# Performance work log

Measured on AMD Instinct MI355X. Metric: run time of the kernel, lower is better.

## Reference

```python
import jax, jax.numpy as jnp
import numpy as np
from jax.ops import segment_sum, segment_max

G_GRAPHS = 64  # number of graphs for global_mean_pool
H_ATTN = 4     # GPSConv global attention heads


def _bn(h, g, b, eps=1e-5):
    # BatchNorm1d over nodes, training-mode (biased) batch statistics
    mu = h.mean(0)
    var = ((h - mu) ** 2).mean(0)
    return (h - mu) * jax.lax.rsqrt(var + eps) * g + b


def _forward(x, edge_index, batch, pre_w1, pre_b1, pre_w2, pre_b2,
             gat_wl, gat_bl, gat_wr, gat_br, gat_att, gat_bias,
             attn_in_w, attn_in_b, attn_out_w, attn_out_b,
             bn1_g, bn1_b, bn2_g, bn2_b, bn3_g, bn3_b,
             mlp_w1, mlp_b1, mlp_w2, mlp_b2, fin_w, fin_b):
    N = x.shape[0]
    L = gat_wl.shape[0]
    loops = jnp.arange(N)
    src = jnp.concatenate([edge_index[0], loops])  # GATv2Conv add_self_loops=True
    dst = jnp.concatenate([edge_index[1], loops])

    # preprocess MLP (exact GELU, as torch.nn.GELU default)
    x = jax.nn.gelu(x @ pre_w1 + pre_b1, approximate=False)
    x = jax.nn.gelu(x @ pre_w2 + pre_b2, approximate=False)

    for l in range(L):
        D = x.shape[1]
        dh = D // H_ATTN
        # ---- local GATv2Conv (heads=1, concat) ----
        xl = x @ gat_wl[l] + gat_bl[l]  # source transform
        xr = x @ gat_wr[l] + gat_br[l]  # target transform
        e = jax.nn.leaky_relu(xl[src] + xr[dst], 0.2) @ gat_att[l]  # [E]
        m = segment_max(e, dst, num_segments=N)
        a = jnp.exp(e - m[dst])
        s = segment_sum(a, dst, num_segments=N)
        alpha = a / s[dst]
        h1 = segment_sum(alpha[:, None] * xl[src], dst, num_segments=N) + gat_bias[l]
        h1 = _bn(h1 + x, bn1_g[l], bn1_b[l])  # residual + norm1
        # ---- global multi-head self-attention over all N nodes (batch=None) ----
        qkv = x @ attn_in_w[l].T + attn_in_b[l]
        q, k, v = jnp.split(qkv, 3, axis=-1)
        q = q.reshape(N, H_ATTN, dh).transpose(1, 0, 2)  # [H,N,dh]
        k = k.reshape(N, H_ATTN, dh).transpose(1, 0, 2)
        v = v.reshape(N, H_ATTN, dh).transpose(1, 0, 2)
        probs = jax.nn.softmax(jnp.einsum('hnd,hmd->hnm', q, k) / np.sqrt(dh), axis=-1)
        o = jnp.einsum('hnm,hmd->hnd', probs, v).transpose(1, 0, 2).reshape(N, D)
        h2 = o @ attn_out_w[l].T + attn_out_b[l]
        h2 = _bn(h2 + x, bn2_g[l], bn2_b[l])  # residual + norm2
        # ---- combine + MLP + norm3 ----
        out = h1 + h2
        out = out + (jax.nn.relu(out @ mlp_w1[l] + mlp_b1[l]) @ mlp_w2[l] + mlp_b2[l])
        out = _bn(out, bn3_g[l], bn3_b[l])
        x = jax.nn.relu(out)  # outer F.relu; dropout is identity in eval

    # global_mean_pool
    sums = segment_sum(x, batch, num_segments=G_GRAPHS)
    cnt = jnp.maximum(segment_sum(jnp.ones((N,), x.dtype), batch, num_segments=G_GRAPHS), 1.0)
    logits = (sums / cnt[:, None]) @ fin_w + fin_b
    return jax.nn.log_softmax(logits, axis=-1)


def setup_inputs() -> dict:
    N, E, F_IN, D, C, L = 4096, 262144, 9, 64, 10, 3
    key = jax.random.key(0)
    ks = iter(jax.random.split(key, 64))
    def nrm(shape, fan):
        return jax.random.normal(next(ks), shape, jnp.float32) / np.sqrt(fan)
    def zeros(shape):
        return jnp.zeros(shape, jnp.float32)
    x = jax.random.normal(next(ks), (N, F_IN), jnp.float32)
    edge_index = jax.random.randint(next(ks), (2, E), 0, N)
    batch = jnp.sort(jax.random.randint(next(ks), (N,), 0, G_GRAPHS))
    return dict(
        x=x, edge_index=edge_index, batch=batch,
        pre_w1=nrm((F_IN, 2 * D), F_IN), pre_b1=zeros((2 * D,)),
        pre_w2=nrm((2 * D, D), 2 * D), pre_b2=zeros((D,)),
        gat_wl=nrm((L, D, D), D), gat_bl=zeros((L, D)),
        gat_wr=nrm((L, D, D), D), gat_br=zeros((L, D)),
        gat_att=nrm((L, D), D), gat_bias=zeros((L, D)),
        attn_in_w=nrm((L, 3 * D, D), D), attn_in_b=zeros((L, 3 * D)),
        attn_out_w=nrm((L, D, D), D), attn_out_b=zeros((L, D)),
        bn1_g=jnp.ones((L, D), jnp.float32), bn1_b=zeros((L, D)),
        bn2_g=jnp.ones((L, D), jnp.float32), bn2_b=zeros((L, D)),
        bn3_g=jnp.ones((L, D), jnp.float32), bn3_b=zeros((L, D)),
        mlp_w1=nrm((L, D, 2 * D), D), mlp_b1=zeros((L, 2 * D)),
        mlp_w2=nrm((L, 2 * D, D), 2 * D), mlp_b2=zeros((L, D)),
        fin_w=nrm((D, C), D), fin_b=zeros((C,)),
    )


def reference(x, edge_index, batch, pre_w1, pre_b1, pre_w2, pre_b2,
              gat_wl, gat_bl, gat_wr, gat_br, gat_att, gat_bias,
              attn_in_w, attn_in_b, attn_out_w, attn_out_b,
              bn1_g, bn1_b, bn2_g, bn2_b, bn3_g, bn3_b,
              mlp_w1, mlp_b1, mlp_w2, mlp_b2, fin_w, fin_b):
    return _forward(x, edge_index, batch, pre_w1, pre_b1, pre_w2, pre_b2,
                    gat_wl, gat_bl, gat_wr, gat_br, gat_att, gat_bias,
                    attn_in_w, attn_in_b, attn_out_w, attn_out_b,
                    bn1_g, bn1_b, bn2_g, bn2_b, bn3_g, bn3_b,
                    mlp_w1, mlp_b1, mlp_w2, mlp_b2, fin_w, fin_b)
```

## Files before the change

kernel.cpp:

```cpp
#include <hip/hip_runtime.h>
#include <math.h>

#define N_NODE 4096
#define N_EDGE 262144
#define E_TOT (N_EDGE + N_NODE)
#define DD 64
#define NL 3
#define NG 64

typedef __fp16 h2_t __attribute__((ext_vector_type(2)));
union H2x4 { uint4 u; h2_t h[4]; };

__device__ __forceinline__ void atomAddF(float* p, float v) {
#if defined(__HIP_PLATFORM_AMD__)
  unsafeAtomicAdd(p, v);
#else
  atomicAdd(p, v);
#endif
}

__global__ void csr_count_kernel(const int* __restrict__ ei, int* __restrict__ cnt) {
  int e = blockIdx.x * blockDim.x + threadIdx.x;
  if (e >= E_TOT) return;
  int dst = (e < N_EDGE) ? ei[N_EDGE + e] : (e - N_EDGE);
  atomicAdd(&cnt[dst], 1);
}

__global__ void csr_scan_kernel(const int* __restrict__ cnt, int* __restrict__ row_ptr,
                                int* __restrict__ nextp) {
  __shared__ int ps[256];
  __shared__ int ps2[257];
  int t = threadIdx.x;
  int base = t * 16;
  int loc[16];
  int s = 0;
#pragma unroll
  for (int k = 0; k < 16; ++k) { loc[k] = s; s += cnt[base + k]; }
  ps[t] = s;
  __syncthreads();
  if (t == 0) {
    int a = 0;
    for (int u = 0; u < 256; ++u) { ps2[u] = a; a += ps[u]; }
    ps2[256] = a;
  }
  __syncthreads();
  int off = ps2[t];
#pragma unroll
  for (int k = 0; k < 16; ++k) {
    int v = off + loc[k];
    row_ptr[base + k] = v;
    nextp[base + k] = v;
  }
  if (t == 0) row_ptr[N_NODE] = ps2[256];
}

__global__ void csr_fill_kernel(const int* __restrict__ ei, int* __restrict__ nextp,
                                int* __restrict__ csr_src) {
  int e = blockIdx.x * blockDim.x + threadIdx.x;
  if (e >= E_TOT) return;
  int src, dst;
  if (e < N_EDGE) { src = ei[e]; dst = ei[N_EDGE + e]; }
  else { src = dst = e - N_EDGE; }
  int pos = atomicAdd(&nextp[dst], 1);
  csr_src[pos] = src;
}

__global__ void build_w_kernel(const float* __restrict__ wl, const float* __restrict__ bl,
                               const float* __restrict__ wr, const float* __restrict__ br,
                               const float* __restrict__ win, const float* __restrict__ bin,
                               const float* __restrict__ wout,
                               float* __restrict__ cw, float* __restrict__ cbias,
                               float* __restrict__ tout) {
  int idx = blockIdx.x * blockDim.x + threadIdx.x;
  if (idx < NL * 64 * 320) {
    int l = idx / 20480, rem = idx % 20480;
    int k = rem / 320, j = rem % 320;
    float v;
    if (j < 64) v = wl[l * 4096 + k * 64 + j];
    else if (j < 128) v = wr[l * 4096 + k * 64 + (j - 64)];
    else v = win[l * 12288 + (j - 128) * 64 + k];
    cw[idx] = v;
  }
  if (idx < NL * 320) {
    int l = idx / 320, j = idx % 320;
    float v;
    if (j < 64) v = bl[l * 64 + j];
    else if (j < 128) v = br[l * 64 + (j - 64)];
    else v = bin[l * 192 + (j - 128)];
    cbias[idx] = v;
  }
  if (idx < NL * 4096) {
    int l = idx / 4096, rem = idx % 4096;
    int k = rem / 64, j = rem % 64;
    tout[l * 4096 + k * 64 + j] = wout[l * 4096 + j * 64 + k];
  }
}

__global__ void linear_kernel(const float* __restrict__ A, const float* __restrict__ W,
                              const float* __restrict__ bias, float* __restrict__ C,
                              float* __restrict__ C2, int split,
                              const float* __restrict__ resid,
                              int K, int Nc, int act) {
  extern __shared__ float sA[];
  int R = blockDim.x / Nc;
  int r = threadIdx.x / Nc;
  int j = threadIdx.x - r * Nc;
  int row0 = blockIdx.x * R;
  for (int idx = threadIdx.x; idx < R * K; idx += blockDim.x)
    sA[idx] = A[row0 * K + idx];
  __syncthreads();
  int row = row0 + r;
  const float* a = sA + r * K;
  float acc = bias[j];
#pragma unroll 8
  for (int k = 0; k < K; ++k) acc = fmaf(a[k], W[k * Nc + j], acc);
  if (act == 1) acc = 0.5f * acc * (1.0f + erff(acc * 0.70710678118654752f));
  else if (act == 2) acc = fmaxf(acc, 0.0f);
  if (resid) acc += resid[row * Nc + j];
  if (j < split) C[row * split + j] = acc;
  else C2[row * (Nc - split) + (j - split)] = acc;
}

__global__ void gat_agg_kernel(const float* __restrict__ x, const float* __restrict__ xlr,
                               const float* __restrict__ att, const float* __restrict__ gbias,
                               const int* __restrict__ row_ptr, const int* __restrict__ csr_src,
                               float* __restrict__ z1) {
  int wave = (blockIdx.x * blockDim.x + threadIdx.x) >> 6;
  int lane = threadIdx.x & 63;
  if (wave >= N_NODE) return;
  int i = wave;
  float xr_d = xlr[i * 128 + 64 + lane];
  float att_d = att[lane];
  float m = -INFINITY, s = 0.f, acc = 0.f;
  int e0 = row_ptr[i], e1 = row_ptr[i + 1];
  for (int e = e0; e < e1; ++e) {
    int src = csr_src[e];
    float xl_d = xlr[src * 128 + lane];
    float v = xl_d + xr_d;
    float lr = (v > 0.f) ? v : 0.2f * v;
    float p = lr * att_d;
#pragma unroll
    for (int off = 32; off; off >>= 1) p += __shfl_xor(p, off, 64);
    float nm = fmaxf(m, p);
    float corr = __expf(m - nm);
    float w = __expf(p - nm);
    s = s * corr + w;
    acc = acc * corr + w * xl_d;
    m = nm;
  }
  z1[i * DD + lane] = x[i * DD + lane] + gbias[lane] + acc / s;
}

__global__ void colstats_kernel(const float* __restrict__ z, float* __restrict__ stats) {
  int d = threadIdx.x & 63;
  int rg = threadIdx.x >> 6;
  int i0 = blockIdx.x * 128;
  float s = 0.f, q = 0.f;
  for (int i = i0 + rg; i < i0 + 128; i += 4) {
    float v = z[i * DD + d];
    s += v;
    q += v * v;
  }
  atomAddF(&stats[d], s);
  atomAddF(&stats[64 + d], q);
}

__global__ void bn_apply_kernel(const float* __restrict__ z, const float* __restrict__ stats,
                                const float* __restrict__ g, const float* __restrict__ b,
                                float* __restrict__ out, int relu) {
  int idx = blockIdx.x * blockDim.x + threadIdx.x;
  if (idx >= N_NODE * DD) return;
  int d = idx & 63;
  const float invN = 1.0f / (float)N_NODE;
  float mu = stats[d] * invN;
  float var = stats[64 + d] * invN - mu * mu;
  float rstd = rsqrtf(var + 1e-5f);
  float v = (z[idx] - mu) * rstd * g[d] + b[d];
  if (relu) v = fmaxf(v, 0.f);
  out[idx] = v;
}

__global__ void bnbn_kernel(const float* __restrict__ z1, const float* __restrict__ st1,
                            const float* __restrict__ g1, const float* __restrict__ b1,
                            const float* __restrict__ z2, const float* __restrict__ st2,
                            const float* __restrict__ g2, const float* __restrict__ b2,
                            float* __restrict__ comb) {
  int idx = blockIdx.x * blockDim.x + threadIdx.x;
  if (idx >= N_NODE * DD) return;
  int d = idx & 63;
  const float invN = 1.0f / (float)N_NODE;
  float mu1 = st1[d] * invN;
  float v1 = st1[64 + d] * invN - mu1 * mu1;
  float h1 = (z1[idx] - mu1) * rsqrtf(v1 + 1e-5f) * g1[d] + b1[d];
  float mu2 = st2[d] * invN;
  float v2 = st2[64 + d] * invN - mu2 * mu2;
  float h2 = (z2[idx] - mu2) * rsqrtf(v2 + 1e-5f) * g2[d] + b2[d];
  comb[idx] = h1 + h2;
}

__global__ void knorm_kernel(const float* __restrict__ qkv, int* __restrict__ kmax) {
  __shared__ int lmax[4];
  int tid = threadIdx.x;
  if (tid < 4) lmax[tid] = 0;
  __syncthreads();
  int idx = blockIdx.x * 256 + tid;
  int j = idx >> 2, h = idx & 3;
  const float* kr = qkv + (size_t)j * 192 + 64 + h * 16;
  float n2 = 0.f;
#pragma unroll
  for (int c = 0; c < 16; ++c) { float v = kr[c]; n2 = fmaf(v, v, n2); }
  atomicMax(&lmax[h], __float_as_int(sqrtf(n2)));
  __syncthreads();
  if (tid < 4) atomicMax(&kmax[tid], lmax[tid]);
}

#define TJ 256
__global__ void attn_kernel(const float* __restrict__ qkv, const int* __restrict__ kmax,
                            float* __restrict__ accS, float* __restrict__ accO) {
  __shared__ __align__(16) float smem[4416];
  uint4* kt = (uint4*)smem;
  uint4* vt = (uint4*)(smem + 2048);
  int h = blockIdx.y, js = blockIdx.z;
  int i0 = blockIdx.x * 64;
  int r = threadIdx.x & 63;
  int gq = threadIdx.x >> 6;
  int i = i0 + r;
  float qf[16];
  const float* qr = qkv + (size_t)i * 192 + h * 16;
#pragma unroll
  for (int c = 0; c < 16; ++c) qf[c] = qr[c] * 0.25f;
  float qn2 = 0.f;
#pragma unroll
  for (int c = 0; c < 16; ++c) qn2 = fmaf(qf[c], qf[c], qn2);
  float m = sqrtf(qn2) * __int_as_float(kmax[h]);
  h2_t q2[8];
#pragma unroll
  for (int c = 0; c < 8; ++c) q2[c] = __builtin_amdgcn_cvt_pkrtz(qf[2 * c], qf[2 * c + 1]);
  float s = 0.f;
  float acc[16];
#pragma unroll
  for (int c = 0; c < 16; ++c) acc[c] = 0.f;

  for (int t = 0; t < 2; ++t) {
    int j0 = js * 512 + t * TJ;
    __syncthreads();
    {
      int jj = threadIdx.x;
      const float* kr = qkv + (size_t)(j0 + jj) * 192 + 64 + h * 16;
      float4 a = *(const float4*)kr, b = *(const float4*)(kr + 4);
      float4 c4f = *(const float4*)(kr + 8), d4 = *(const float4*)(kr + 12);
      H2x4 w0, w1;
      w0.h[0] = __builtin_amdgcn_cvt_pkrtz(a.x, a.y); w0.h[1] = __builtin_amdgcn_cvt_pkrtz(a.z, a.w);
      w0.h[2] = __builtin_amdgcn_cvt_pkrtz(b.x, b.y); w0.h[3] = __builtin_amdgcn_cvt_pkrtz(b.z, b.w);
      w1.h[0] = __builtin_amdgcn_cvt_pkrtz(c4f.x, c4f.y); w1.h[1] = __builtin_amdgcn_cvt_pkrtz(c4f.z, c4f.w);
      w1.h[2] = __builtin_amdgcn_cvt_pkrtz(d4.x, d4.y); w1.h[3] = __builtin_amdgcn_cvt_pkrtz(d4.z, d4.w);
      kt[jj * 2] = w0.u; kt[jj * 2 + 1] = w1.u;
      for (int id = threadIdx.x; id < 512; id += 256) {
        int c4 = id & 3, jp = id >> 2;
        const float* va = qkv + (size_t)(j0 + 2 * jp) * 192 + 128 + h * 16 + c4 * 4;
        float4 A = *(const float4*)va, B = *(const float4*)(va + 192);
        H2x4 w;
        w.h[0] = __builtin_amdgcn_cvt_pkrtz(A.x, B.x); w.h[1] = __builtin_amdgcn_cvt_pkrtz(A.y, B.y);
        w.h[2] = __builtin_amdgcn_cvt_pkrtz(A.z, B.z); w.h[3] = __builtin_amdgcn_cvt_pkrtz(A.w, B.w);
        vt[c4 * 128 + jp] = w.u;
      }
    }
    __syncthreads();
    for (int jp = gq; jp < 128; jp += 4) {
      H2x4 ka0, ka1, kb0, kb1;
      ka0.u = kt[jp * 4 + 0]; ka1.u = kt[jp * 4 + 1];
      kb0.u = kt[jp * 4 + 2]; kb1.u = kt[jp * 4 + 3];
      float sa = 0.f, sb = 0.f;
#pragma unroll
      for (int c = 0; c < 4; ++c) {
        sa = __builtin_amdgcn_fdot2(q2[c], ka0.h[c], sa, false);
        sb = __builtin_amdgcn_fdot2(q2[c], kb0.h[c], sb, false);
      }
#pragma unroll
      for (int c = 0; c < 4; ++c) {
        sa = __builtin_amdgcn_fdot2(q2[4 + c], ka1.h[c], sa, false);
        sb = __builtin_amdgcn_fdot2(q2[4 + c], kb1.h[c], sb, false);
      }
      float pa = __expf(sa - m), pb = __expf(sb - m);
      s += pa + pb;
      h2_t pp = __builtin_amdgcn_cvt_pkrtz(pa, pb);
      H2x4 v0, v1, v2, v3;
      v0.u = vt[jp]; v1.u = vt[128 + jp]; v2.u = vt[256 + jp]; v3.u = vt[384 + jp];
#pragma unroll
      for (int c = 0; c < 4; ++c) {
        acc[c]      = __builtin_amdgcn_fdot2(pp, v0.h[c], acc[c], false);
        acc[4 + c]  = __builtin_amdgcn_fdot2(pp, v1.h[c], acc[4 + c], false);
        acc[8 + c]  = __builtin_amdgcn_fdot2(pp, v2.h[c], acc[8 + c], false);
        acc[12 + c] = __builtin_amdgcn_fdot2(pp, v3.h[c], acc[12 + c], false);
      }
    }
  }
  __syncthreads();
  float* cb = smem;
  cb[(gq * 17 + 16) * 64 + r] = s;
#pragma unroll
  for (int c = 0; c < 16; ++c) cb[(gq * 17 + c) * 64 + r] = acc[c];
  __syncthreads();
  if (gq == 0) {
    float S = 0.f;
#pragma unroll
    for (int g2 = 0; g2 < 4; ++g2) S += cb[(g2 * 17 + 16) * 64 + r];
    atomAddF(&accS[h * N_NODE + i], S);
#pragma unroll
    for (int c = 0; c < 16; ++c) {
      float A = 0.f;
#pragma unroll
      for (int g2 = 0; g2 < 4; ++g2) A += cb[(g2 * 17 + c) * 64 + r];
      atomAddF(&accO[(h * 16 + c) * N_NODE + i], A);
    }
  }
}

__global__ void attn_norm_kernel(float* __restrict__ accO, float* __restrict__ accS,
                                 int* __restrict__ kmax, float* __restrict__ o) {
  int idx = blockIdx.x * 256 + threadIdx.x;
  int i = idx >> 6, d = idx & 63, h = d >> 4;
  o[idx] = accO[d * N_NODE + i] / accS[h * N_NODE + i];
  __syncthreads();
  accO[d * N_NODE + i] = 0.f;
  if ((d & 15) == 0) accS[h * N_NODE + i] = 0.f;
  if (idx < 4) kmax[idx] = 0;
}

__global__ void pool_kernel(const float* __restrict__ x, const int* __restrict__ batch,
                            float* __restrict__ pool, float* __restrict__ pcnt) {
  int idx = blockIdx.x * blockDim.x + threadIdx.x;
  if (idx >= N_NODE * DD) return;
  int i = idx >> 6, d = idx & 63;
  int g = batch[i];
  atomAddF(&pool[g * DD + d], x[idx]);
  if (d == 0) atomAddF(&pcnt[g], 1.0f);
}

__global__ void final_kernel(const float* __restrict__ pool, const float* __restrict__ pcnt,
                             const float* __restrict__ fw, const float* __restrict__ fb,
                             float* __restrict__ out) {
  int g = blockIdx.x;
  int d = threadIdx.x;
  __shared__ float mean[64];
  __shared__ float lg[16];
  float c = fmaxf(pcnt[g], 1.0f);
  mean[d] = pool[g * DD + d] / c;
  __syncthreads();
  if (d < 10) {
    float acc = fb[d];
#pragma unroll 8
    for (int k = 0; k < 64; ++k) acc += mean[k] * fw[k * 10 + d];
    lg[d] = acc;
  }
  __syncthreads();
  if (d == 0) {
    float mx = -INFINITY;
    for (int c2 = 0; c2 < 10; ++c2) mx = fmaxf(mx, lg[c2]);
    float sum = 0.f;
    for (int c2 = 0; c2 < 10; ++c2) sum += expf(lg[c2] - mx);
    lg[10] = mx + logf(sum);
  }
  __syncthreads();
  if (d < 10) out[g * 10 + d] = lg[d] - lg[10];
}

static void run_linear(const float* A, const float* W, const float* b, float* C,
                       float* C2, int split, const float* resid,
                       int K, int Nc, int act, int R, hipStream_t s) {
  int block = Nc * R;
  int grid = N_NODE / R;
  hipLaunchKernelGGL(linear_kernel, dim3(grid), dim3(block), R * K * sizeof(float), s,
                     A, W, b, C, C2, split, resid, K, Nc, act);
}

extern "C" void kernel_launch(void* const* d_in, const int* in_sizes, int n_in,
                              void* d_out, int out_size, void* d_ws, size_t ws_size,
                              hipStream_t stream) {
  const float* x_in      = (const float*)d_in[0];
  const int*   edge_idx  = (const int*)d_in[1];
  const int*   batch     = (const int*)d_in[2];
  const float* pre_w1    = (const float*)d_in[3];
  const float* pre_b1    = (const float*)d_in[4];
  const float* pre_w2    = (const float*)d_in[5];
  const float* pre_b2    = (const float*)d_in[6];
  const float* gat_wl    = (const float*)d_in[7];
  const float* gat_bl    = (const float*)d_in[8];
  const float* gat_wr    = (const float*)d_in[9];
  const float* gat_br    = (const float*)d_in[10];
  const float* gat_att   = (const float*)d_in[11];
  const float* gat_bias  = (const float*)d_in[12];
  const float* attn_in_w = (const float*)d_in[13];
  const float* attn_in_b = (const float*)d_in[14];
  const float* attn_out_w= (const float*)d_in[15];
  const float* attn_out_b= (const float*)d_in[16];
  const float* bn1_g     = (const float*)d_in[17];
  const float* bn1_b     = (const float*)d_in[18];
  const float* bn2_g     = (const float*)d_in[19];
  const float* bn2_b     = (const float*)d_in[20];
  const float* bn3_g     = (const float*)d_in[21];
  const float* bn3_b     = (const float*)d_in[22];
  const float* mlp_w1    = (const float*)d_in[23];
  const float* mlp_b1    = (const float*)d_in[24];
  const float* mlp_w2    = (const float*)d_in[25];
  const float* mlp_b2    = (const float*)d_in[26];
  const float* fin_w     = (const float*)d_in[27];
  const float* fin_b     = (const float*)d_in[28];
  float* out = (float*)d_out;

  float* ws = (float*)d_ws;
  float* xbuf  = ws;
  float* qkv   = xbuf + 262144;
  float* xlr   = qkv + 786432;
  float* hid   = xlr + 524288;
  float* obuf  = hid;
  float* z1    = hid + 262144;
  float* z2    = hid + 524288;
  float* comb  = z2 + 262144;
  float* cw    = comb + 262144;
  float* cbias = cw + 61440;
  float* tout  = cbias + 960;
  float* zr    = tout + 12288;
  int*   cnt   = (int*)zr;
  float* stats = zr + 4096;
  float* pool  = stats + 1152;
  float* pcnt  = pool + 4096;
  int*   kmax  = (int*)(pcnt + 64);
  float* accS  = (float*)(kmax + 4);
  float* accO  = accS + 16384;
  size_t zr_elems = 4096 + 1152 + 4096 + 64 + 4 + 16384 + 262144;
  float* zend  = accO + 262144;
  int* row_ptr = (int*)zend;
  int* nextp   = row_ptr + 4097;
  int* csr_src = nextp + 4096;

  hipMemsetAsync(zr, 0, zr_elems * sizeof(float), stream);

  hipLaunchKernelGGL(csr_count_kernel, dim3((E_TOT + 255) / 256), dim3(256), 0, stream,
                     edge_idx, cnt);
  hipLaunchKernelGGL(csr_scan_kernel, dim3(1), dim3(256), 0, stream, cnt, row_ptr, nextp);
  hipLaunchKernelGGL(csr_fill_kernel, dim3((E_TOT + 255) / 256), dim3(256), 0, stream,
                     edge_idx, nextp, csr_src);

  hipLaunchKernelGGL(build_w_kernel, dim3((NL * 64 * 320 + 255) / 256), dim3(256), 0, stream,
                     gat_wl, gat_bl, gat_wr, gat_br, attn_in_w, attn_in_b, attn_out_w,
                     cw, cbias, tout);

  run_linear(x_in, pre_w1, pre_b1, xlr, nullptr, 128, nullptr, 9, 128, 1, 2, stream);
  run_linear(xlr, pre_w2, pre_b2, xbuf, nullptr, 64, nullptr, 128, 64, 1, 4, stream);

  for (int l = 0; l < NL; ++l) {
    const float* attv = gat_att + l * DD;
    const float* gbias = gat_bias + l * DD;
    float* st1 = stats + (l * 3 + 0) * 128;
    float* st2 = stats + (l * 3 + 1) * 128;
    float* st3 = stats + (l * 3 + 2) * 128;

    run_linear(xbuf, cw + l * 20480, cbias + l * 320, xlr, qkv, 128, nullptr,
               64, 320, 0, 2, stream);

    hipLaunchKernelGGL(knorm_kernel, dim3(64), dim3(256), 0, stream, qkv, kmax);
    hipLaunchKernelGGL(attn_kernel, dim3(N_NODE / 64, 4, 8), dim3(256), 0, stream,
                       qkv, kmax, accS, accO);
    hipLaunchKernelGGL(attn_norm_kernel, dim3(N_NODE * DD / 256), dim3(256), 0, stream,
                       accO, accS, kmax, obuf);

    hipLaunchKernelGGL(gat_agg_kernel, dim3(N_NODE / 4), dim3(256), 0, stream,
                       xbuf, xlr, attv, gbias, row_ptr, csr_src, z1);
    hipLaunchKernelGGL(colstats_kernel, dim3(32), dim3(256), 0, stream, z1, st1);

    run_linear(obuf, tout + l * 4096, attn_out_b + l * DD, z2, nullptr, 64, xbuf,
               64, 64, 0, 4, stream);
    hipLaunchKernelGGL(colstats_kernel, dim3(32), dim3(256), 0, stream, z2, st2);

    hipLaunchKernelGGL(bnbn_kernel, dim3(N_NODE * DD / 256), dim3(256), 0, stream,
                       z1, st1, bn1_g + l * DD, bn1_b + l * DD,
                       z2, st2, bn2_g + l * DD, bn2_b + l * DD, comb);

    run_linear(comb, mlp_w1 + l * 8192, mlp_b1 + l * 128, hid, nullptr, 128, nullptr,
               64, 128, 2, 2, stream);
    run_linear(hid, mlp_w2 + l * 8192, mlp_b2 + l * DD, z2, nullptr, 64, comb,
               128, 64, 0, 4, stream);
    hipLaunchKernelGGL(colstats_kernel, dim3(32), dim3(256), 0, stream, z2, st3);
    hipLaunchKernelGGL(bn_apply_kernel, dim3(N_NODE * DD / 256), dim3(256), 0, stream,
                       z2, st3, bn3_g + l * DD, bn3_b + l * DD, xbuf, 1);
  }

  hipLaunchKernelGGL(pool_kernel, dim3(N_NODE * DD / 256), dim3(256), 0, stream,
                     xbuf, batch, pool, pcnt);
  hipLaunchKernelGGL(final_kernel, dim3(NG), dim3(64), 0, stream, pool, pcnt, fin_w, fin_b, out);
}
```

Measured before the change: 769.8 us.

## Fuse batchnorm, stats and attention normalization into templated linear kernels

Replaces the generic linear kernel with a templated one that keeps weights in registers and processes 16 rows per block. BatchNorm application is folded into the input loads and residual adds of the following linears. Column statistics become per-block partial sums plus a small reduction kernel, and the attention normalization and accumulator clearing move into the output projection. This cuts launches and full-tensor round trips through memory, at the cost of more template variants, register pressure from large weight arrays, and recomputing BN per consumer.

Measured after the change: 1.801 ms. 2.34x slower.

```diff
diff --git a/kernel.cpp b/kernel.cpp
--- a/kernel.cpp
+++ b/kernel.cpp
@@ -17,6 +17,16 @@
 #else
   atomicAdd(p, v);
 #endif
+}
+
+__device__ __forceinline__ float bn_eval(float z, const float* st, const float* g,
+                                         const float* b, int d, bool relu) {
+  if (st == nullptr) return z;
+  const float invN = 2.44140625e-4f;
+  float mu = st[d] * invN;
+  float var = fmaf(st[64 + d], invN, -mu * mu);
+  float v = (z - mu) * rsqrtf(var + 1e-5f) * g[d] + b[d];
+  return relu ? fmaxf(v, 0.f) : v;
 }
 
 __global__ void csr_count_kernel(const int* __restrict__ ei, int* __restrict__ cnt) {
@@ -96,39 +106,140 @@
   }
 }
 
-__global__ void linear_kernel(const float* __restrict__ A, const float* __restrict__ W,
-                              const float* __restrict__ bias, float* __restrict__ C,
-                              float* __restrict__ C2, int split,
-                              const float* __restrict__ resid,
-                              int K, int Nc, int act) {
-  extern __shared__ float sA[];
-  int R = blockDim.x / Nc;
-  int r = threadIdx.x / Nc;
-  int j = threadIdx.x - r * Nc;
-  int row0 = blockIdx.x * R;
-  for (int idx = threadIdx.x; idx < R * K; idx += blockDim.x)
-    sA[idx] = A[row0 * K + idx];
-  __syncthreads();
-  int row = row0 + r;
-  const float* a = sA + r * K;
-  float acc = bias[j];
-#pragma unroll 8
-  for (int k = 0; k < K; ++k) acc = fmaf(a[k], W[k * Nc + j], acc);
-  if (act == 1) acc = 0.5f * acc * (1.0f + erff(acc * 0.70710678118654752f));
-  else if (act == 2) acc = fmaxf(acc, 0.0f);
-  if (resid) acc += resid[row * Nc + j];
-  if (j < split) C[row * split + j] = acc;
-  else C2[row * (Nc - split) + (j - split)] = acc;
-}
-
-__global__ void gat_agg_kernel(const float* __restrict__ x, const float* __restrict__ xlr,
-                               const float* __restrict__ att, const float* __restrict__ gbias,
-                               const int* __restrict__ row_ptr, const int* __restrict__ csr_src,
-                               float* __restrict__ z1) {
-  int wave = (blockIdx.x * blockDim.x + threadIdx.x) >> 6;
-  int lane = threadIdx.x & 63;
-  if (wave >= N_NODE) return;
-  int i = wave;
+struct LinP {
+  const float *A, *A2, *W, *bias;
+  float *C, *C2;
+  const float *i_st, *i_g, *i_b, *i2_st, *i2_g, *i2_b;
+  const float *R, *R2, *r_st, *r_g, *r_b, *r2_st, *r2_g, *r2_b;
+  float *accO_w, *accS_w;
+  int* kmax_clr;
+  float* spart;
+};
+
+template<int NC, int KK, int TIN, int TRES, int ACT, bool SPLIT, bool STOUT, bool KCLR>
+__global__ void lin_kernel(LinP P) {
+  constexpr int BLK = (NC < 256) ? 256 : NC;
+  constexpr int G = BLK / NC;
+  constexpr int BR = 16;
+  constexpr int RPT = BR / G;
+  constexpr int LDA = (KK % 4 == 0) ? KK + 4 : KK;
+  __shared__ __align__(16) float sA[BR * LDA];
+  __shared__ float sred[4 * 128];
+  const int tid = threadIdx.x;
+  const int row0 = blockIdx.x * BR;
+
+  for (int idx = tid; idx < BR * KK; idx += BLK) {
+    int r, k;
+    if constexpr (TIN == 3) { r = idx & 15; k = idx >> 4; }
+    else { r = idx / KK; k = idx - r * KK; }
+    int row = row0 + r;
+    float v;
+    if constexpr (TIN == 0) v = P.A[row * KK + k];
+    else if constexpr (TIN == 1) v = bn_eval(P.A[row * 64 + k], P.i_st, P.i_g, P.i_b, k, true);
+    else if constexpr (TIN == 2) v = bn_eval(P.A[row * 64 + k], P.i_st, P.i_g, P.i_b, k, false)
+                                   + bn_eval(P.A2[row * 64 + k], P.i2_st, P.i2_g, P.i2_b, k, false);
+    else {
+      float num = P.accO_w[k * 4096 + row];
+      float den = P.accS_w[(k >> 4) * 4096 + row];
+      v = num / den;
+      P.accO_w[k * 4096 + row] = 0.f;
+    }
+    sA[r * LDA + k] = v;
+  }
+  if constexpr (KCLR) { if (blockIdx.x == 0 && tid < 4) P.kmax_clr[tid] = 0; }
+
+  int j, rg;
+  if constexpr (G == 1) { j = tid; rg = 0; }
+  else { j = tid & (NC - 1); rg = tid >> (NC == 64 ? 6 : 7); }
+
+  float w[KK];
+#pragma unroll
+  for (int k = 0; k < KK; ++k) w[k] = P.W[k * NC + j];
+  float bs = P.bias[j];
+  float acc[RPT];
+#pragma unroll
+  for (int rr = 0; rr < RPT; ++rr) acc[rr] = bs;
+  __syncthreads();
+
+  if constexpr (TIN == 3) {
+    if (tid < 64) P.accS_w[(tid >> 4) * 4096 + row0 + (tid & 15)] = 0.f;
+  }
+
+  if constexpr (KK % 4 == 0) {
+#pragma unroll
+    for (int rr = 0; rr < RPT; ++rr) {
+      const float* ap = sA + (rg * RPT + rr) * LDA;
+#pragma unroll
+      for (int k4 = 0; k4 < KK / 4; ++k4) {
+        float4 a = *(const float4*)(ap + 4 * k4);
+        acc[rr] = fmaf(a.x, w[4 * k4 + 0], acc[rr]);
+        acc[rr] = fmaf(a.y, w[4 * k4 + 1], acc[rr]);
+        acc[rr] = fmaf(a.z, w[4 * k4 + 2], acc[rr]);
+        acc[rr] = fmaf(a.w, w[4 * k4 + 3], acc[rr]);
+      }
+    }
+  } else {
+#pragma unroll
+    for (int rr = 0; rr < RPT; ++rr) {
+      const float* ap = sA + (rg * RPT + rr) * LDA;
+#pragma unroll
+      for (int k = 0; k < KK; ++k) acc[rr] = fmaf(ap[k], w[k], acc[rr]);
+    }
+  }
+
+  float lsum = 0.f, lsq = 0.f;
+#pragma unroll
+  for (int rr = 0; rr < RPT; ++rr) {
+    int row = row0 + rg * RPT + rr;
+    float v = acc[rr];
+    if constexpr (ACT == 1) v = 0.5f * v * (1.0f + erff(v * 0.70710678118654752f));
+    else if constexpr (ACT == 2) v = fmaxf(v, 0.0f);
+    if constexpr (TRES == 1) v += bn_eval(P.R[row * 64 + j], P.r_st, P.r_g, P.r_b, j, true);
+    else if constexpr (TRES == 2) v += bn_eval(P.R[row * 64 + j], P.r_st, P.r_g, P.r_b, j, false)
+                                     + bn_eval(P.R2[row * 64 + j], P.r2_st, P.r2_g, P.r2_b, j, false);
+    if constexpr (SPLIT) {
+      if (j < 128) P.C[row * 128 + j] = v;
+      else P.C2[row * 192 + (j - 128)] = v;
+    } else {
+      P.C[row * NC + j] = v;
+    }
+    if constexpr (STOUT) { lsum += v; lsq = fmaf(v, v, lsq); }
+  }
+  if constexpr (STOUT) {
+    sred[rg * 128 + j] = lsum;
+    sred[rg * 128 + 64 + j] = lsq;
+    __syncthreads();
+    if (rg == 0) {
+      float s0 = 0.f, q0 = 0.f;
+#pragma unroll
+      for (int g2 = 0; g2 < G; ++g2) { s0 += sred[g2 * 128 + j]; q0 += sred[g2 * 128 + 64 + j]; }
+      P.spart[blockIdx.x * 128 + j] = s0;
+      P.spart[blockIdx.x * 128 + 64 + j] = q0;
+    }
+  }
+}
+
+__global__ void red_kernel(const float* __restrict__ p1, float* __restrict__ s1,
+                           const float* __restrict__ p2, float* __restrict__ s2) {
+  const float* p = blockIdx.y ? p2 : p1;
+  float* s = blockIdx.y ? s2 : s1;
+  int c = blockIdx.x;
+  float a = 0.f;
+  for (int bb = threadIdx.x; bb < 256; bb += 64) a += p[bb * 128 + c];
+#pragma unroll
+  for (int off = 32; off; off >>= 1) a += __shfl_xor(a, off, 64);
+  if (threadIdx.x == 0) s[c] = a;
+}
+
+__global__ __launch_bounds__(1024) void gat_agg_kernel(
+    const float* __restrict__ state, const float* __restrict__ st3,
+    const float* __restrict__ g3, const float* __restrict__ b3,
+    const float* __restrict__ xlr, const float* __restrict__ att,
+    const float* __restrict__ gbias, const int* __restrict__ row_ptr,
+    const int* __restrict__ csr_src, float* __restrict__ z1, float* __restrict__ spart) {
+  __shared__ float red[16][64];
+  int w = threadIdx.x >> 6, lane = threadIdx.x & 63;
+  int i = blockIdx.x * 16 + w;
   float xr_d = xlr[i * 128 + 64 + lane];
   float att_d = att[lane];
   float m = -INFINITY, s = 0.f, acc = 0.f;
@@ -136,66 +247,30 @@
   for (int e = e0; e < e1; ++e) {
     int src = csr_src[e];
     float xl_d = xlr[src * 128 + lane];
-    float v = xl_d + xr_d;
-    float lr = (v > 0.f) ? v : 0.2f * v;
+    float vv = xl_d + xr_d;
+    float lr = (vv > 0.f) ? vv : 0.2f * vv;
     float p = lr * att_d;
 #pragma unroll
     for (int off = 32; off; off >>= 1) p += __shfl_xor(p, off, 64);
     float nm = fmaxf(m, p);
     float corr = __expf(m - nm);
-    float w = __expf(p - nm);
-    s = s * corr + w;
-    acc = acc * corr + w * xl_d;
+    float wt = __expf(p - nm);
+    s = s * corr + wt;
+    acc = acc * corr + wt * xl_d;
     m = nm;
   }
-  z1[i * DD + lane] = x[i * DD + lane] + gbias[lane] + acc / s;
-}
-
-__global__ void colstats_kernel(const float* __restrict__ z, float* __restrict__ stats) {
-  int d = threadIdx.x & 63;
-  int rg = threadIdx.x >> 6;
-  int i0 = blockIdx.x * 128;
-  float s = 0.f, q = 0.f;
-  for (int i = i0 + rg; i < i0 + 128; i += 4) {
-    float v = z[i * DD + d];
-    s += v;
-    q += v * v;
-  }
-  atomAddF(&stats[d], s);
-  atomAddF(&stats[64 + d], q);
-}
-
-__global__ void bn_apply_kernel(const float* __restrict__ z, const float* __restrict__ stats,
-                                const float* __restrict__ g, const float* __restrict__ b,
-                                float* __restrict__ out, int relu) {
-  int idx = blockIdx.x * blockDim.x + threadIdx.x;
-  if (idx >= N_NODE * DD) return;
-  int d = idx & 63;
-  const float invN = 1.0f / (float)N_NODE;
-  float mu = stats[d] * invN;
-  float var = stats[64 + d] * invN - mu * mu;
-  float rstd = rsqrtf(var + 1e-5f);
-  float v = (z[idx] - mu) * rstd * g[d] + b[d];
-  if (relu) v = fmaxf(v, 0.f);
-  out[idx] = v;
-}
-
-__global__ void bnbn_kernel(const float* __restrict__ z1, const float* __restrict__ st1,
-                            const float* __restrict__ g1, const float* __restrict__ b1,
-                            const float* __restrict__ z2, const float* __restrict__ st2,
-                            const float* __restrict__ g2, const float* __restrict__ b2,
-                            float* __restrict__ comb) {
-  int idx = blockIdx.x * blockDim.x + threadIdx.x;
-  if (idx >= N_NODE * DD) return;
-  int d = idx & 63;
-  const float invN = 1.0f / (float)N_NODE;
-  float mu1 = st1[d] * invN;
-  float v1 = st1[64 + d] * invN - mu1 * mu1;
-  float h1 = (z1[idx] - mu1) * rsqrtf(v1 + 1e-5f) * g1[d] + b1[d];
-  float mu2 = st2[d] * invN;
-  float v2 = st2[64 + d] * invN - mu2 * mu2;
-  float h2 = (z2[idx] - mu2) * rsqrtf(v2 + 1e-5f) * g2[d] + b2[d];
-  comb[idx] = h1 + h2;
+  float resid = bn_eval(state[i * 64 + lane], st3, g3, b3, lane, true);
+  float val = resid + gbias[lane] + acc / s;
+  z1[i * 64 + lane] = val;
+  red[w][lane] = val;
+  __syncthreads();
+  if (w == 0) {
+    float ss = 0.f, qq = 0.f;
+#pragma unroll
+    for (int u = 0; u < 16; ++u) { float v = red[u][lane]; ss += v; qq = fmaf(v, v, qq); }
+    spart[blockIdx.x * 128 + lane] = ss;
+    spart[blockIdx.x * 128 + 64 + lane] = qq;
+  }
 }
 
 __global__ void knorm_kernel(const float* __restrict__ qkv, int* __restrict__ kmax) {
@@ -316,25 +391,17 @@
   }
 }
 
-__global__ void attn_norm_kernel(float* __restrict__ accO, float* __restrict__ accS,
-                                 int* __restrict__ kmax, float* __restrict__ o) {
-  int idx = blockIdx.x * 256 + threadIdx.x;
-  int i = idx >> 6, d = idx & 63, h = d >> 4;
-  o[idx] = accO[d * N_NODE + i] / accS[h * N_NODE + i];
-  __syncthreads();
-  accO[d * N_NODE + i] = 0.f;
-  if ((d & 15) == 0) accS[h * N_NODE + i] = 0.f;
-  if (idx < 4) kmax[idx] = 0;
-}
-
-__global__ void pool_kernel(const float* __restrict__ x, const int* __restrict__ batch,
-                            float* __restrict__ pool, float* __restrict__ pcnt) {
+__global__ void pool_kernel(const float* __restrict__ z3, const float* __restrict__ st,
+                            const float* __restrict__ g, const float* __restrict__ b,
+                            const int* __restrict__ batch, float* __restrict__ pool,
+                            float* __restrict__ pcnt) {
   int idx = blockIdx.x * blockDim.x + threadIdx.x;
   if (idx >= N_NODE * DD) return;
   int i = idx >> 6, d = idx & 63;
-  int g = batch[i];
-  atomAddF(&pool[g * DD + d], x[idx]);
-  if (d == 0) atomAddF(&pcnt[g], 1.0f);
+  float v = bn_eval(z3[idx], st, g, b, d, true);
+  int gg = batch[i];
+  atomAddF(&pool[gg * DD + d], v);
+  if (d == 0) atomAddF(&pcnt[gg], 1.0f);
 }
 
 __global__ void final_kernel(const float* __restrict__ pool, const float* __restrict__ pcnt,
@@ -363,15 +430,6 @@
   }
   __syncthreads();
   if (d < 10) out[g * 10 + d] = lg[d] - lg[10];
-}
-
-static void run_linear(const float* A, const float* W, const float* b, float* C,
-                       float* C2, int split, const float* resid,
-                       int K, int Nc, int act, int R, hipStream_t s) {
-  int block = Nc * R;
-  int grid = N_NODE / R;
-  hipLaunchKernelGGL(linear_kernel, dim3(grid), dim3(block), R * K * sizeof(float), s,
-                     A, W, b, C, C2, split, resid, K, Nc, act);
 }
 
 extern "C" void kernel_launch(void* const* d_in, const int* in_sizes, int n_in,
@@ -408,27 +466,32 @@
   const float* fin_b     = (const float*)d_in[28];
   float* out = (float*)d_out;
 
-  float* ws = (float*)d_ws;
+  float* ws    = (float*)d_ws;
   float* xbuf  = ws;
-  float* qkv   = xbuf + 262144;
-  float* xlr   = qkv + 786432;
-  float* hid   = xlr + 524288;
-  float* obuf  = hid;
-  float* z1    = hid + 262144;
-  float* z2    = hid + 524288;
-  float* comb  = z2 + 262144;
-  float* cw    = comb + 262144;
+  float* xlr   = xbuf + 262144;
+  float* qkv   = xlr + 524288;
+  float* hid   = qkv;
+  float* z1    = qkv + 786432;
+  float* z2    = z1 + 262144;
+  float* zA    = z2 + 262144;
+  float* zB    = zA + 262144;
+  float* cw    = zB + 262144;
   float* cbias = cw + 61440;
   float* tout  = cbias + 960;
-  float* zr    = tout + 12288;
+  float* st1   = tout + 12288;
+  float* st2   = st1 + 128;
+  float* st3   = st2 + 128;
+  float* st1p  = st3 + 128;
+  float* st3p  = st1p;
+  float* st2p  = st1p + 32768;
+  float* zr    = st2p + 32768;
   int*   cnt   = (int*)zr;
-  float* stats = zr + 4096;
-  float* pool  = stats + 1152;
+  float* pool  = zr + 4096;
   float* pcnt  = pool + 4096;
   int*   kmax  = (int*)(pcnt + 64);
   float* accS  = (float*)(kmax + 4);
   float* accO  = accS + 16384;
-  size_t zr_elems = 4096 + 1152 + 4096 + 64 + 4 + 16384 + 262144;
+  size_t zr_elems = 4096 + 4096 + 64 + 4 + 16384 + 262144;
   float* zend  = accO + 262144;
   int* row_ptr = (int*)zend;
   int* nextp   = row_ptr + 4097;
@@ -446,47 +509,72 @@
                      gat_wl, gat_bl, gat_wr, gat_br, attn_in_w, attn_in_b, attn_out_w,
                      cw, cbias, tout);
 
-  run_linear(x_in, pre_w1, pre_b1, xlr, nullptr, 128, nullptr, 9, 128, 1, 2, stream);
-  run_linear(xlr, pre_w2, pre_b2, xbuf, nullptr, 64, nullptr, 128, 64, 1, 4, stream);
+  {
+    LinP p = {}; p.A = x_in; p.W = pre_w1; p.bias = pre_b1; p.C = xlr;
+    hipLaunchKernelGGL((lin_kernel<128, 9, 0, 0, 1, false, false, false>),
+                       dim3(256), dim3(256), 0, stream, p);
+  }
+  {
+    LinP p = {}; p.A = xlr; p.W = pre_w2; p.bias = pre_b2; p.C = xbuf;
+    hipLaunchKernelGGL((lin_kernel<64, 128, 0, 0, 1, false, false, false>),
+                       dim3(256), dim3(256), 0, stream, p);
+  }
+
+  const float* state = xbuf;
+  const float* sstat = nullptr;
+  const float* sg = nullptr;
+  const float* sb = nullptr;
 
   for (int l = 0; l < NL; ++l) {
-    const float* attv = gat_att + l * DD;
-    const float* gbias = gat_bias + l * DD;
-    float* st1 = stats + (l * 3 + 0) * 128;
-    float* st2 = stats + (l * 3 + 1) * 128;
-    float* st3 = stats + (l * 3 + 2) * 128;
-
-    run_linear(xbuf, cw + l * 20480, cbias + l * 320, xlr, qkv, 128, nullptr,
-               64, 320, 0, 2, stream);
-
+    float* zcur = (l & 1) ? zB : zA;
+
+    {
+      LinP p = {}; p.A = state; p.W = cw + l * 20480; p.bias = cbias + l * 320;
+      p.C = xlr; p.C2 = qkv;
+      p.i_st = sstat; p.i_g = sg; p.i_b = sb;
+      hipLaunchKernelGGL((lin_kernel<320, 64, 1, 0, 0, true, false, false>),
+                         dim3(256), dim3(320), 0, stream, p);
+    }
     hipLaunchKernelGGL(knorm_kernel, dim3(64), dim3(256), 0, stream, qkv, kmax);
     hipLaunchKernelGGL(attn_kernel, dim3(N_NODE / 64, 4, 8), dim3(256), 0, stream,
                        qkv, kmax, accS, accO);
-    hipLaunchKernelGGL(attn_norm_kernel, dim3(N_NODE * DD / 256), dim3(256), 0, stream,
-                       accO, accS, kmax, obuf);
-
-    hipLaunchKernelGGL(gat_agg_kernel, dim3(N_NODE / 4), dim3(256), 0, stream,
-                       xbuf, xlr, attv, gbias, row_ptr, csr_src, z1);
-    hipLaunchKernelGGL(colstats_kernel, dim3(32), dim3(256), 0, stream, z1, st1);
-
-    run_linear(obuf, tout + l * 4096, attn_out_b + l * DD, z2, nullptr, 64, xbuf,
-               64, 64, 0, 4, stream);
-    hipLaunchKernelGGL(colstats_kernel, dim3(32), dim3(256), 0, stream, z2, st2);
-
-    hipLaunchKernelGGL(bnbn_kernel, dim3(N_NODE * DD / 256), dim3(256), 0, stream,
-                       z1, st1, bn1_g + l * DD, bn1_b + l * DD,
-                       z2, st2, bn2_g + l * DD, bn2_b + l * DD, comb);
-
-    run_linear(comb, mlp_w1 + l * 8192, mlp_b1 + l * 128, hid, nullptr, 128, nullptr,
-               64, 128, 2, 2, stream);
-    run_linear(hid, mlp_w2 + l * 8192, mlp_b2 + l * DD, z2, nullptr, 64, comb,
-               128, 64, 0, 4, stream);
-    hipLaunchKernelGGL(colstats_kernel, dim3(32), dim3(256), 0, stream, z2, st3);
-    hipLaunchKernelGGL(bn_apply_kernel, dim3(N_NODE * DD / 256), dim3(256), 0, stream,
-                       z2, st3, bn3_g + l * DD, bn3_b + l * DD, xbuf, 1);
+    hipLaunchKernelGGL(gat_agg_kernel, dim3(256), dim3(1024), 0, stream,
+                       state, sstat, sg, sb, xlr, gat_att + l * DD, gat_bias + l * DD,
+                       row_ptr, csr_src, z1, st1p);
+    {
+      LinP p = {}; p.W = tout + l * 4096; p.bias = attn_out_b + l * DD; p.C = z2;
+      p.accO_w = accO; p.accS_w = accS; p.kmax_clr = kmax;
+      p.R = state; p.r_st = sstat; p.r_g = sg; p.r_b = sb;
+      p.spart = st2p;
+      hipLaunchKernelGGL((lin_kernel<64, 64, 3, 1, 0, false, true, true>),
+                         dim3(256), dim3(256), 0, stream, p);
+    }
+    hipLaunchKernelGGL(red_kernel, dim3(128, 2), dim3(64), 0, stream, st1p, st1, st2p, st2);
+    {
+      LinP p = {}; p.A = z1; p.A2 = z2; p.W = mlp_w1 + l * 8192; p.bias = mlp_b1 + l * 128;
+      p.C = hid;
+      p.i_st = st1; p.i_g = bn1_g + l * DD; p.i_b = bn1_b + l * DD;
+      p.i2_st = st2; p.i2_g = bn2_g + l * DD; p.i2_b = bn2_b + l * DD;
+      hipLaunchKernelGGL((lin_kernel<128, 64, 2, 0, 2, false, false, false>),
+                         dim3(256), dim3(256), 0, stream, p);
+    }
+    {
+      LinP p = {}; p.A = hid; p.W = mlp_w2 + l * 8192; p.bias = mlp_b2 + l * DD; p.C = zcur;
+      p.R = z1; p.r_st = st1; p.r_g = bn1_g + l * DD; p.r_b = bn1_b + l * DD;
+      p.R2 = z2; p.r2_st = st2; p.r2_g = bn2_g + l * DD; p.r2_b = bn2_b + l * DD;
+      p.spart = st3p;
+      hipLaunchKernelGGL((lin_kernel<64, 128, 0, 2, 0, false, true, false>),
+                         dim3(256), dim3(256), 0, stream, p);
+    }
+    hipLaunchKernelGGL(red_kernel, dim3(128, 1), dim3(64), 0, stream, st3p, st3, st2p, st2);
+
+    state = zcur;
+    sstat = st3;
+    sg = bn3_g + l * DD;
+    sb = bn3_b + l * DD;
   }
 
   hipLaunchKernelGGL(pool_kernel, dim3(N_NODE * DD / 256), dim3(256), 0, stream,
-                     xbuf, batch, pool, pcnt);
+                     state, sstat, sg, sb, batch, pool, pcnt);
   hipLaunchKernelGGL(final_kernel, dim3(NG), dim3(64), 0, stream, pool, pcnt, fin_w, fin_b, out);
 }
```
